# Kernel optimization log

Hardware: AMD Instinct MI355X
Metric: run time of the kernel (lower is better)

Reference implementation:

```python
import jax, jax.numpy as jnp
import numpy as np

B, T = 1024, 200
V = 100000   # item_size
H = 256      # hidden_size == embedding_size (GRU consumes embedding directly)
NUM_LAYERS = 2


def _gru_layer(x, w_ih, w_hh):
    """PyTorch GRU layer, bias=False. x: [B,T,in], w_ih: [3H,in], w_hh: [3H,H].
    Gate order in weights is (r, z, n)."""
    h0 = jnp.zeros((x.shape[0], w_hh.shape[1]), x.dtype)
    # Precompute all input projections in one big GEMM: [B,T,3H]
    x_proj = jnp.einsum('bti,gi->btg', x, w_ih)

    def step(h, xp):
        hp = h @ w_hh.T                      # [B,3H]
        xr, xz, xn = jnp.split(xp, 3, axis=-1)
        hr, hz, hn = jnp.split(hp, 3, axis=-1)
        r = jax.nn.sigmoid(xr + hr)
        z = jax.nn.sigmoid(xz + hz)
        n = jnp.tanh(xn + r * hn)
        h_new = (1.0 - z) * n + z * h
        return h_new, h_new

    _, ys = jax.lax.scan(step, h0, jnp.swapaxes(x_proj, 0, 1))  # [T,B,H]
    return jnp.swapaxes(ys, 0, 1)  # [B,T,H]


def setup_inputs() -> dict:
    key = jax.random.key(0)
    ks = jax.random.split(key, 8)
    input_ids = jax.random.randint(ks[0], (B, T), 0, V)
    s = 0.05
    emb = jax.random.normal(ks[1], (V, H), jnp.float32) * s
    emb = emb.at[0].set(0.0)  # padding_idx=0
    w_ih_l0 = jax.random.normal(ks[2], (3 * H, H), jnp.float32) * s
    w_hh_l0 = jax.random.normal(ks[3], (3 * H, H), jnp.float32) * s
    w_ih_l1 = jax.random.normal(ks[4], (3 * H, H), jnp.float32) * s
    w_hh_l1 = jax.random.normal(ks[5], (3 * H, H), jnp.float32) * s
    dense_w = jax.random.normal(ks[6], (H, H), jnp.float32) * s  # Linear(H, E=H)
    dense_b = jax.random.normal(ks[7], (H,), jnp.float32) * s
    return {"input_ids": input_ids, "emb": emb,
            "w_ih_l0": w_ih_l0, "w_hh_l0": w_hh_l0,
            "w_ih_l1": w_ih_l1, "w_hh_l1": w_hh_l1,
            "dense_w": dense_w, "dense_b": dense_b}


def reference(input_ids, emb, w_ih_l0, w_hh_l0, w_ih_l1, w_hh_l1, dense_w, dense_b):
    x = emb[input_ids]                 # [B,T,H] embedding lookup
    # emb_dropout is identity in eval mode
    x = _gru_layer(x, w_ih_l0, w_hh_l0)
    x = _gru_layer(x, w_ih_l1, w_hh_l1)
    return x @ dense_w.T + dense_b     # [B,T,H]
```

## Files before the change

### kernel.cpp

```cpp
#include <hip/hip_runtime.h>

#define T_LEN 200
#define HID   256
#define BATCH 1024
#define G3    768
#define ROWS  16
#define NTHREADS 512
#define WSZ   196608

typedef __bf16  bf16x8 __attribute__((ext_vector_type(8)));
typedef float   f32x4  __attribute__((ext_vector_type(4)));

__device__ __forceinline__ unsigned short f2bf(float f) {
  union { float f; unsigned int u; } c; c.f = f;
  unsigned int u = c.u;
  u += 0x7FFFu + ((u >> 16) & 1u);
  return (unsigned short)(u >> 16);
}
__device__ __forceinline__ float bf2f(unsigned int u16v) {
  union { unsigned int u; float f; } c; c.u = u16v << 16; return c.f;
}
__device__ __forceinline__ float sigm(float x) { return 1.0f / (1.0f + __expf(-x)); }
__device__ __forceinline__ float tanh_f(float x) { return 1.0f - 2.0f / (__expf(2.0f * x) + 1.0f); }

__global__ void convert_weights(const float* __restrict__ a,
                                const float* __restrict__ b,
                                const float* __restrict__ c,
                                const float* __restrict__ d,
                                const float* __restrict__ e,
                                unsigned short* __restrict__ out) {
  int i = blockIdx.x * blockDim.x + threadIdx.x;
  const int total = 4 * WSZ + HID * HID;
  if (i >= total) return;
  float v;
  if      (i < 1 * WSZ) v = a[i];
  else if (i < 2 * WSZ) v = b[i - 1 * WSZ];
  else if (i < 3 * WSZ) v = c[i - 2 * WSZ];
  else if (i < 4 * WSZ) v = d[i - 3 * WSZ];
  else                  v = e[i - 4 * WSZ];
  out[i] = f2bf(v);
}

__device__ __forceinline__ bf16x8 lds_frag(const unsigned short* buf, int row, int k, int lq) {
  int chunk = (k << 2) + lq;
  int idx = row * HID + ((chunk ^ (row & 7)) << 3);
  return *reinterpret_cast<const bf16x8*>(buf + idx);
}
__device__ __forceinline__ bf16x8 gw_frag(const unsigned short* __restrict__ W, int wrow, int kof) {
  return *reinterpret_cast<const bf16x8*>(W + (size_t)wrow * HID + kof);
}
__device__ __forceinline__ uint2 pack4(f32x4 v) {
  uint2 r;
  r.x = (unsigned int)f2bf(v[0]) | ((unsigned int)f2bf(v[1]) << 16);
  r.y = (unsigned int)f2bf(v[2]) | ((unsigned int)f2bf(v[3]) << 16);
  return r;
}

template<int GATHER>
__global__ __launch_bounds__(NTHREADS)
void xp_gemm(const int* __restrict__ ids, const float* __restrict__ emb,
             const unsigned short* __restrict__ hsrc,
             const unsigned short* __restrict__ W,
             unsigned short* __restrict__ xpT)
{
  __shared__ __align__(16) unsigned short As[128 * HID];
  const int tid = threadIdx.x;
  const int w = tid >> 6, lane = tid & 63, lr = lane & 15, lq = lane >> 4;
  const int bt = blockIdx.x & 63;
  const int tt = blockIdx.x >> 6;
  const int r0 = bt * 16, t0 = tt * 8;

  for (int idx = tid; idx < 128 * 32; idx += NTHREADS) {
    int row = idx >> 5, cc = idx & 31;
    int bloc = row & 15, tloc = row >> 4;
    int sidx = row * HID + ((cc ^ (row & 7)) << 3);
    if (GATHER) {
      int rid = ids[(r0 + bloc) * T_LEN + t0 + tloc];
      const f32x4* src = reinterpret_cast<const f32x4*>(emb + (size_t)rid * HID + cc * 8);
      f32x4 v0 = src[0], v1 = src[1];
      uint4 pk;
      pk.x = (unsigned int)f2bf(v0[0]) | ((unsigned int)f2bf(v0[1]) << 16);
      pk.y = (unsigned int)f2bf(v0[2]) | ((unsigned int)f2bf(v0[3]) << 16);
      pk.z = (unsigned int)f2bf(v1[0]) | ((unsigned int)f2bf(v1[1]) << 16);
      pk.w = (unsigned int)f2bf(v1[2]) | ((unsigned int)f2bf(v1[3]) << 16);
      *reinterpret_cast<uint4*>(&As[sidx]) = pk;
    } else {
      uint4 v = *reinterpret_cast<const uint4*>(hsrc + ((size_t)(r0 + bloc) * T_LEN + t0 + tloc) * HID + cc * 8);
      *reinterpret_cast<uint4*>(&As[sidx]) = v;
    }
  }
  __syncthreads();

  const int colbase = w * 96;
  #pragma unroll 1
  for (int mt = 0; mt < 8; ++mt) {
    bf16x8 a[8];
    #pragma unroll
    for (int k = 0; k < 8; ++k) a[k] = lds_frag(As, mt * 16 + lr, k, lq);
    const int t = t0 + mt;
    unsigned short* xprow = xpT + ((size_t)t * 64 + bt) * (G3 * 16);
    #pragma unroll
    for (int np = 0; np < 3; ++np) {
      const int c0 = colbase + np * 32;
      f32x4 acc0 = {0,0,0,0}, acc1 = {0,0,0,0};
      #pragma unroll
      for (int k = 0; k < 8; ++k) {
        const int kof = k * 32 + lq * 8;
        bf16x8 b0 = gw_frag(W, c0 + lr,      kof);
        bf16x8 b1 = gw_frag(W, c0 + 16 + lr, kof);
        acc0 = __builtin_amdgcn_mfma_f32_16x16x32_bf16(a[k], b0, acc0, 0, 0, 0);
        acc1 = __builtin_amdgcn_mfma_f32_16x16x32_bf16(a[k], b1, acc1, 0, 0, 0);
      }
      *reinterpret_cast<uint2*>(xprow + (c0 + lr)      * 16 + lq * 4) = pack4(acc0);
      *reinterpret_cast<uint2*>(xprow + (c0 + 16 + lr) * 16 + lq * 4) = pack4(acc1);
    }
  }
}

__global__ __launch_bounds__(NTHREADS, 2)
void gru_rec(const unsigned short* __restrict__ xpT,
             const unsigned short* __restrict__ Whh,
             unsigned short* __restrict__ hout)
{
  __shared__ __align__(16) unsigned short hb[2][ROWS * HID];
  const int tid = threadIdx.x;
  const int w = tid >> 6, lane = tid & 63, lr = lane & 15, lq = lane >> 4;
  const int bt = blockIdx.x;
  const int r0 = bt * ROWS;
  const int c0 = w * 32;

  bf16x8 wf[2][3][8];
  #pragma unroll
  for (int j = 0; j < 2; ++j)
    #pragma unroll
    for (int g = 0; g < 3; ++g)
      #pragma unroll
      for (int k = 0; k < 8; ++k)
        wf[j][g][k] = gw_frag(Whh, g * 256 + c0 + j * 16 + lr, k * 32 + lq * 8);

  for (int i = tid; i < ROWS * HID; i += NTHREADS) { hb[0][i] = 0; }

  f32x4 hreg[2] = {{0,0,0,0},{0,0,0,0}};

  const int bj0 = (c0 + lr) * 16 + lq * 4;
  const int bj1 = (c0 + 16 + lr) * 16 + lq * 4;

  const size_t slabstep = (size_t)64 * G3 * 16;
  const unsigned short* slab = xpT + (size_t)bt * (G3 * 16);

  __syncthreads();

  uint2 pz[2][3];
  #pragma unroll
  for (int g = 0; g < 3; ++g) {
    pz[0][g] = *reinterpret_cast<const uint2*>(slab + g * 4096 + bj0);
    pz[1][g] = *reinterpret_cast<const uint2*>(slab + g * 4096 + bj1);
  }

  int cur = 0;
  for (int t = 0; t < T_LEN; ++t) {
    f32x4 acc[2][3];
    uint2 xn0 = pz[0][2], xn1 = pz[1][2];
    #pragma unroll
    for (int j = 0; j < 2; ++j) {
      #pragma unroll
      for (int g = 0; g < 2; ++g) {
        uint2 p = pz[j][g];
        f32x4 v;
        v[0] = bf2f(p.x & 0xffffu); v[1] = bf2f(p.x >> 16);
        v[2] = bf2f(p.y & 0xffffu); v[3] = bf2f(p.y >> 16);
        acc[j][g] = v;
      }
      f32x4 z4 = {0,0,0,0};
      acc[j][2] = z4;
    }

    {
      const unsigned short* slab2 = (t + 1 < T_LEN) ? slab + slabstep : slab;
      #pragma unroll
      for (int g = 0; g < 3; ++g) {
        pz[0][g] = *reinterpret_cast<const uint2*>(slab2 + g * 4096 + bj0);
        pz[1][g] = *reinterpret_cast<const uint2*>(slab2 + g * 4096 + bj1);
      }
    }

    asm volatile("s_waitcnt lgkmcnt(0)\n\ts_barrier" ::: "memory");

    #pragma unroll
    for (int k = 0; k < 8; ++k) {
      bf16x8 a = lds_frag(hb[cur], lr, k, lq);
      #pragma unroll
      for (int j = 0; j < 2; ++j) {
        acc[j][0] = __builtin_amdgcn_mfma_f32_16x16x32_bf16(a, wf[j][0][k], acc[j][0], 0, 0, 0);
        acc[j][1] = __builtin_amdgcn_mfma_f32_16x16x32_bf16(a, wf[j][1][k], acc[j][1], 0, 0, 0);
        acc[j][2] = __builtin_amdgcn_mfma_f32_16x16x32_bf16(a, wf[j][2][k], acc[j][2], 0, 0, 0);
      }
    }

    #pragma unroll
    for (int j = 0; j < 2; ++j) {
      uint2 xn = j ? xn1 : xn0;
      float xnv[4];
      xnv[0] = bf2f(xn.x & 0xffffu); xnv[1] = bf2f(xn.x >> 16);
      xnv[2] = bf2f(xn.y & 0xffffu); xnv[3] = bf2f(xn.y >> 16);
      #pragma unroll
      for (int q = 0; q < 4; ++q) {
        float r = sigm(acc[j][0][q]);
        float z = sigm(acc[j][1][q]);
        float n = tanh_f(xnv[q] + r * acc[j][2][q]);
        float hnew = (1.0f - z) * n + z * hreg[j][q];
        hreg[j][q] = hnew;
        unsigned short hb16 = f2bf(hnew);
        int m = lq * 4 + q;
        int c = c0 + j * 16 + lr;
        hb[cur ^ 1][m * HID + (((c >> 3) ^ (m & 7)) << 3) + (c & 7)] = hb16;
        hout[((size_t)(r0 + m) * T_LEN + t) * HID + c] = hb16;
      }
    }
    slab += slabstep;
    cur ^= 1;
  }
}

__global__ __launch_bounds__(NTHREADS)
void dense_gemm(const unsigned short* __restrict__ hsrc,
                const unsigned short* __restrict__ Wd,
                const float* __restrict__ db,
                float* __restrict__ out)
{
  __shared__ __align__(16) unsigned short As[128 * HID];
  const int tid = threadIdx.x;
  const int w = tid >> 6, lane = tid & 63, lr = lane & 15, lq = lane >> 4;
  const int bt = blockIdx.x & 63;
  const int tt = blockIdx.x >> 6;
  const int r0 = bt * 16, t0 = tt * 8;

  for (int idx = tid; idx < 128 * 32; idx += NTHREADS) {
    int row = idx >> 5, cc = idx & 31;
    int bloc = row & 15, tloc = row >> 4;
    int sidx = row * HID + ((cc ^ (row & 7)) << 3);
    uint4 v = *reinterpret_cast<const uint4*>(hsrc + ((size_t)(r0 + bloc) * T_LEN + t0 + tloc) * HID + cc * 8);
    *reinterpret_cast<uint4*>(&As[sidx]) = v;
  }
  __syncthreads();

  const int c0 = w * 32;
  const float b0v = db[c0 + lr];
  const float b1v = db[c0 + 16 + lr];

  #pragma unroll 1
  for (int mt = 0; mt < 8; ++mt) {
    bf16x8 a[8];
    #pragma unroll
    for (int k = 0; k < 8; ++k) a[k] = lds_frag(As, mt * 16 + lr, k, lq);
    f32x4 acc0 = {0,0,0,0}, acc1 = {0,0,0,0};
    #pragma unroll
    for (int k = 0; k < 8; ++k) {
      const int kof = k * 32 + lq * 8;
      bf16x8 b0 = gw_frag(Wd, c0 + lr,      kof);
      bf16x8 b1 = gw_frag(Wd, c0 + 16 + lr, kof);
      acc0 = __builtin_amdgcn_mfma_f32_16x16x32_bf16(a[k], b0, acc0, 0, 0, 0);
      acc1 = __builtin_amdgcn_mfma_f32_16x16x32_bf16(a[k], b1, acc1, 0, 0, 0);
    }
    const int t = t0 + mt;
    #pragma unroll
    for (int q = 0; q < 4; ++q) {
      size_t base = ((size_t)(r0 + lq * 4 + q) * T_LEN + t) * HID;
      out[base + c0 + lr]      = acc0[q] + b0v;
      out[base + c0 + 16 + lr] = acc1[q] + b1v;
    }
  }
}

__device__ __forceinline__ void layer_step(
    const bf16x8* ax, const bf16x8* ah,
    const unsigned short* __restrict__ Wih,
    const unsigned short* __restrict__ Whh,
    float (&hreg)[2][4],
    unsigned short* __restrict__ outb,
    int c0base, int lr, int lq)
{
  #pragma unroll
  for (int j = 0; j < 2; ++j) {
    const int c0 = c0base + j * 16;
    f32x4 xr = {0,0,0,0}, xz = {0,0,0,0}, xn = {0,0,0,0};
    f32x4 hr = {0,0,0,0}, hz = {0,0,0,0}, hn = {0,0,0,0};
    #pragma unroll
    for (int k = 0; k < 8; ++k) {
      const int kof = k * 32 + lq * 8;
      bf16x8 b0 = gw_frag(Wih,       c0 + lr, kof);
      bf16x8 b1 = gw_frag(Wih, 256 + c0 + lr, kof);
      bf16x8 b2 = gw_frag(Wih, 512 + c0 + lr, kof);
      bf16x8 w0 = gw_frag(Whh,       c0 + lr, kof);
      bf16x8 w1 = gw_frag(Whh, 256 + c0 + lr, kof);
      bf16x8 w2 = gw_frag(Whh, 512 + c0 + lr, kof);
      xr = __builtin_amdgcn_mfma_f32_16x16x32_bf16(ax[k], b0, xr, 0, 0, 0);
      xz = __builtin_amdgcn_mfma_f32_16x16x32_bf16(ax[k], b1, xz, 0, 0, 0);
      xn = __builtin_amdgcn_mfma_f32_16x16x32_bf16(ax[k], b2, xn, 0, 0, 0);
      hr = __builtin_amdgcn_mfma_f32_16x16x32_bf16(ah[k], w0, hr, 0, 0, 0);
      hz = __builtin_amdgcn_mfma_f32_16x16x32_bf16(ah[k], w1, hz, 0, 0, 0);
      hn = __builtin_amdgcn_mfma_f32_16x16x32_bf16(ah[k], w2, hn, 0, 0, 0);
    }
    #pragma unroll
    for (int q = 0; q < 4; ++q) {
      float r = sigm(xr[q] + hr[q]);
      float z = sigm(xz[q] + hz[q]);
      float n = tanh_f(xn[q] + r * hn[q]);
      float h = (1.0f - z) * n + z * hreg[j][q];
      hreg[j][q] = h;
      int m = lq * 4 + q;
      int c = c0 + lr;
      int idx = m * HID + (((c >> 3) ^ (m & 7)) << 3) + (c & 7);
      outb[idx] = f2bf(h);
    }
  }
}

__global__ __launch_bounds__(NTHREADS)
void gru_fused(const int* __restrict__ ids,
               const float* __restrict__ emb,
               const unsigned short* __restrict__ wbf,
               const float* __restrict__ dense_b,
               float* __restrict__ out)
{
  __shared__ __align__(16) unsigned short x_bf[ROWS * HID];
  __shared__ __align__(16) unsigned short h0b[2][ROWS * HID];
  __shared__ __align__(16) unsigned short h1b[2][ROWS * HID];

  const int tid  = threadIdx.x;
  const int w    = tid >> 6;
  const int lane = tid & 63;
  const int lr   = lane & 15;
  const int lq   = lane >> 4;
  const int r0   = blockIdx.x * ROWS;
  const int c0base = w * 32;

  const unsigned short* Wih0 = wbf;
  const unsigned short* Whh0 = wbf + 1 * WSZ;
  const unsigned short* Wih1 = wbf + 2 * WSZ;
  const unsigned short* Whh1 = wbf + 3 * WSZ;
  const unsigned short* Wd   = wbf + 4 * WSZ;

  for (int i = tid; i < ROWS * HID; i += NTHREADS) {
    h0b[0][i] = 0; h0b[1][i] = 0; h1b[0][i] = 0; h1b[1][i] = 0;
  }
  float hreg0[2][4] = {}; float hreg1[2][4] = {};
  const float bias0 = dense_b[c0base + lr];
  const float bias1 = dense_b[c0base + 16 + lr];

  const int grow   = tid >> 5;
  const int gchunk = tid & 31;
  const int gswz   = grow * HID + ((gchunk ^ (grow & 7)) << 3);
  const int gid_base = (r0 + grow) * T_LEN;

  __syncthreads();

  int cur = 0;
  for (int t = 0; t < T_LEN; ++t) {
    {
      int rid = ids[gid_base + t];
      const f32x4* src = reinterpret_cast<const f32x4*>(emb + (size_t)rid * HID + gchunk * 8);
      f32x4 v0 = src[0];
      f32x4 v1 = src[1];
      uint4 pk;
      pk.x = (unsigned int)f2bf(v0[0]) | ((unsigned int)f2bf(v0[1]) << 16);
      pk.y = (unsigned int)f2bf(v0[2]) | ((unsigned int)f2bf(v0[3]) << 16);
      pk.z = (unsigned int)f2bf(v1[0]) | ((unsigned int)f2bf(v1[1]) << 16);
      pk.w = (unsigned int)f2bf(v1[2]) | ((unsigned int)f2bf(v1[3]) << 16);
      *reinterpret_cast<uint4*>(&x_bf[gswz]) = pk;
    }
    __syncthreads();

    bf16x8 ax[8], ah[8];
    #pragma unroll
    for (int k = 0; k < 8; ++k) {
      ax[k] = lds_frag(x_bf,     lr, k, lq);
      ah[k] = lds_frag(h0b[cur], lr, k, lq);
    }
    layer_step(ax, ah, Wih0, Whh0, hreg0, h0b[cur ^ 1], c0base, lr, lq);
    __syncthreads();

    #pragma unroll
    for (int k = 0; k < 8; ++k) {
      ax[k] = lds_frag(h0b[cur ^ 1], lr, k, lq);
      ah[k] = lds_frag(h1b[cur],     lr, k, lq);
    }
    layer_step(ax, ah, Wih1, Whh1, hreg1, h1b[cur ^ 1], c0base, lr, lq);
    __syncthreads();

    #pragma unroll
    for (int k = 0; k < 8; ++k) ax[k] = lds_frag(h1b[cur ^ 1], lr, k, lq);
    #pragma unroll
    for (int j = 0; j < 2; ++j) {
      const int c0 = c0base + j * 16;
      f32x4 acc = {0,0,0,0};
      #pragma unroll
      for (int k = 0; k < 8; ++k) {
        bf16x8 bw = gw_frag(Wd, c0 + lr, k * 32 + lq * 8);
        acc = __builtin_amdgcn_mfma_f32_16x16x32_bf16(ax[k], bw, acc, 0, 0, 0);
      }
      const float bias = j ? bias1 : bias0;
      size_t base = ((size_t)(r0 + lq * 4) * T_LEN + t) * HID + c0 + lr;
      #pragma unroll
      for (int q = 0; q < 4; ++q) {
        out[base + (size_t)q * T_LEN * HID] = acc[q] + bias;
      }
    }
    cur ^= 1;
  }
}

extern "C" void kernel_launch(void* const* d_in, const int* in_sizes, int n_in,
                              void* d_out, int out_size, void* d_ws, size_t ws_size,
                              hipStream_t stream) {
  const int*   ids  = (const int*)d_in[0];
  const float* emb  = (const float*)d_in[1];
  const float* wih0 = (const float*)d_in[2];
  const float* whh0 = (const float*)d_in[3];
  const float* wih1 = (const float*)d_in[4];
  const float* whh1 = (const float*)d_in[5];
  const float* dw   = (const float*)d_in[6];
  const float* db   = (const float*)d_in[7];

  unsigned short* wbf = (unsigned short*)d_ws;

  const int total = 4 * WSZ + HID * HID;
  convert_weights<<<(total + 255) / 256, 256, 0, stream>>>(wih0, whh0, wih1, whh1, dw, wbf);

  const size_t XP_OFF = 2u * 1024u * 1024u;
  const size_t XP_BYTES = (size_t)T_LEN * G3 * BATCH * 2;
  const size_t H_OFF  = XP_OFF + XP_BYTES;
  const size_t H_BYTES = (size_t)BATCH * T_LEN * HID * 2;
  const size_t NEED = H_OFF + H_BYTES;

  if (ws_size >= NEED) {
    unsigned short* xpT  = (unsigned short*)((char*)d_ws + XP_OFF);
    unsigned short* hbuf = (unsigned short*)((char*)d_ws + H_OFF);
    const unsigned short* Wih0 = wbf;
    const unsigned short* Whh0 = wbf + 1 * WSZ;
    const unsigned short* Wih1 = wbf + 2 * WSZ;
    const unsigned short* Whh1 = wbf + 3 * WSZ;
    const unsigned short* Wd   = wbf + 4 * WSZ;

    xp_gemm<1><<<1600, NTHREADS, 0, stream>>>(ids, emb, nullptr, Wih0, xpT);
    gru_rec<<<64, NTHREADS, 0, stream>>>(xpT, Whh0, hbuf);
    xp_gemm<0><<<1600, NTHREADS, 0, stream>>>(nullptr, nullptr, hbuf, Wih1, xpT);
    gru_rec<<<64, NTHREADS, 0, stream>>>(xpT, Whh1, hbuf);
    dense_gemm<<<1600, NTHREADS, 0, stream>>>(hbuf, Wd, db, (float*)d_out);
  } else {
    gru_fused<<<64, NTHREADS, 0, stream>>>(ids, emb, wbf, db, (float*)d_out);
  }
}
```

Before: 2.432 ms.

## Split GRU recurrence across 16 waves with one 16-column tile each

The recurrent kernel now runs 1024 threads (16 waves) per block instead of 512, and each wave owns a single 16-column slice of the hidden state rather than two. This halves the per-wave MFMA chain and gate math on the serial per-timestep critical path, and halves the per-wave register footprint for the resident W_hh fragments. An empty asm pins those fragments in VGPRs. In exchange, the per-step barrier has to synchronize twice as many waves. The launch-bounds occupancy hint is also raised.

```diff
diff --git a/kernel.cpp b/kernel.cpp
--- a/kernel.cpp
+++ b/kernel.cpp
@@ -6,6 +6,7 @@
 #define G3    768
 #define ROWS  16
 #define NTHREADS 512
+#define RECTHREADS 1024
 #define WSZ   196608
 
 typedef __bf16  bf16x8 __attribute__((ext_vector_type(8)));
@@ -49,6 +50,10 @@
 __device__ __forceinline__ bf16x8 gw_frag(const unsigned short* __restrict__ W, int wrow, int kof) {
   return *reinterpret_cast<const bf16x8*>(W + (size_t)wrow * HID + kof);
 }
+__device__ __forceinline__ uint4 gw_fragu(const unsigned short* __restrict__ W, int wrow, int kof) {
+  return *reinterpret_cast<const uint4*>(W + (size_t)wrow * HID + kof);
+}
+__device__ __forceinline__ bf16x8 as_bf(uint4 u) { return __builtin_bit_cast(bf16x8, u); }
 __device__ __forceinline__ uint2 pack4(f32x4 v) {
   uint2 r;
   r.x = (unsigned int)f2bf(v[0]) | ((unsigned int)f2bf(v[1]) << 16);
@@ -117,7 +122,7 @@
   }
 }
 
-__global__ __launch_bounds__(NTHREADS, 2)
+__global__ __launch_bounds__(RECTHREADS, 4)
 void gru_rec(const unsigned short* __restrict__ xpT,
              const unsigned short* __restrict__ Whh,
              unsigned short* __restrict__ hout)
@@ -127,61 +132,57 @@
   const int w = tid >> 6, lane = tid & 63, lr = lane & 15, lq = lane >> 4;
   const int bt = blockIdx.x;
   const int r0 = bt * ROWS;
-  const int c0 = w * 32;
-
-  bf16x8 wf[2][3][8];
+  const int c0 = w * 16;
+
+  uint4 wf[3][8];
   #pragma unroll
-  for (int j = 0; j < 2; ++j)
-    #pragma unroll
-    for (int g = 0; g < 3; ++g)
-      #pragma unroll
-      for (int k = 0; k < 8; ++k)
-        wf[j][g][k] = gw_frag(Whh, g * 256 + c0 + j * 16 + lr, k * 32 + lq * 8);
-
-  for (int i = tid; i < ROWS * HID; i += NTHREADS) { hb[0][i] = 0; }
-
-  f32x4 hreg[2] = {{0,0,0,0},{0,0,0,0}};
-
-  const int bj0 = (c0 + lr) * 16 + lq * 4;
-  const int bj1 = (c0 + 16 + lr) * 16 + lq * 4;
+  for (int g = 0; g < 3; ++g)
+    #pragma unroll
+    for (int k = 0; k < 8; ++k)
+      wf[g][k] = gw_fragu(Whh, g * 256 + c0 + lr, k * 32 + lq * 8);
+  #pragma unroll
+  for (int g = 0; g < 3; ++g)
+    #pragma unroll
+    for (int k = 0; k < 8; ++k)
+      asm volatile("" : "+v"(wf[g][k].x), "+v"(wf[g][k].y),
+                        "+v"(wf[g][k].z), "+v"(wf[g][k].w));
+
+  for (int i = tid; i < ROWS * HID; i += RECTHREADS) { hb[0][i] = 0; }
+
+  f32x4 hreg = {0, 0, 0, 0};
+
+  const int bj = (c0 + lr) * 16 + lq * 4;
 
   const size_t slabstep = (size_t)64 * G3 * 16;
   const unsigned short* slab = xpT + (size_t)bt * (G3 * 16);
 
   __syncthreads();
 
-  uint2 pz[2][3];
+  uint2 pz[3];
   #pragma unroll
-  for (int g = 0; g < 3; ++g) {
-    pz[0][g] = *reinterpret_cast<const uint2*>(slab + g * 4096 + bj0);
-    pz[1][g] = *reinterpret_cast<const uint2*>(slab + g * 4096 + bj1);
-  }
+  for (int g = 0; g < 3; ++g)
+    pz[g] = *reinterpret_cast<const uint2*>(slab + g * 4096 + bj);
 
   int cur = 0;
+  #pragma unroll 1
   for (int t = 0; t < T_LEN; ++t) {
-    f32x4 acc[2][3];
-    uint2 xn0 = pz[0][2], xn1 = pz[1][2];
-    #pragma unroll
-    for (int j = 0; j < 2; ++j) {
-      #pragma unroll
-      for (int g = 0; g < 2; ++g) {
-        uint2 p = pz[j][g];
-        f32x4 v;
-        v[0] = bf2f(p.x & 0xffffu); v[1] = bf2f(p.x >> 16);
-        v[2] = bf2f(p.y & 0xffffu); v[3] = bf2f(p.y >> 16);
-        acc[j][g] = v;
-      }
-      f32x4 z4 = {0,0,0,0};
-      acc[j][2] = z4;
-    }
+    f32x4 acc[3];
+    uint2 xn = pz[2];
+    #pragma unroll
+    for (int g = 0; g < 2; ++g) {
+      uint2 p = pz[g];
+      f32x4 v;
+      v[0] = bf2f(p.x & 0xffffu); v[1] = bf2f(p.x >> 16);
+      v[2] = bf2f(p.y & 0xffffu); v[3] = bf2f(p.y >> 16);
+      acc[g] = v;
+    }
+    { f32x4 z4 = {0,0,0,0}; acc[2] = z4; }
 
     {
       const unsigned short* slab2 = (t + 1 < T_LEN) ? slab + slabstep : slab;
       #pragma unroll
-      for (int g = 0; g < 3; ++g) {
-        pz[0][g] = *reinterpret_cast<const uint2*>(slab2 + g * 4096 + bj0);
-        pz[1][g] = *reinterpret_cast<const uint2*>(slab2 + g * 4096 + bj1);
-      }
+      for (int g = 0; g < 3; ++g)
+        pz[g] = *reinterpret_cast<const uint2*>(slab2 + g * 4096 + bj);
     }
 
     asm volatile("s_waitcnt lgkmcnt(0)\n\ts_barrier" ::: "memory");
@@ -189,30 +190,25 @@
     #pragma unroll
     for (int k = 0; k < 8; ++k) {
       bf16x8 a = lds_frag(hb[cur], lr, k, lq);
-      #pragma unroll
-      for (int j = 0; j < 2; ++j) {
-        acc[j][0] = __builtin_amdgcn_mfma_f32_16x16x32_bf16(a, wf[j][0][k], acc[j][0], 0, 0, 0);
-        acc[j][1] = __builtin_amdgcn_mfma_f32_16x16x32_bf16(a, wf[j][1][k], acc[j][1], 0, 0, 0);
-        acc[j][2] = __builtin_amdgcn_mfma_f32_16x16x32_bf16(a, wf[j][2][k], acc[j][2], 0, 0, 0);
-      }
-    }
-
-    #pragma unroll
-    for (int j = 0; j < 2; ++j) {
-      uint2 xn = j ? xn1 : xn0;
+      acc[0] = __builtin_amdgcn_mfma_f32_16x16x32_bf16(a, as_bf(wf[0][k]), acc[0], 0, 0, 0);
+      acc[1] = __builtin_amdgcn_mfma_f32_16x16x32_bf16(a, as_bf(wf[1][k]), acc[1], 0, 0, 0);
+      acc[2] = __builtin_amdgcn_mfma_f32_16x16x32_bf16(a, as_bf(wf[2][k]), acc[2], 0, 0, 0);
+    }
+
+    {
       float xnv[4];
       xnv[0] = bf2f(xn.x & 0xffffu); xnv[1] = bf2f(xn.x >> 16);
       xnv[2] = bf2f(xn.y & 0xffffu); xnv[3] = bf2f(xn.y >> 16);
+      const int c = c0 + lr;
       #pragma unroll
       for (int q = 0; q < 4; ++q) {
-        float r = sigm(acc[j][0][q]);
-        float z = sigm(acc[j][1][q]);
-        float n = tanh_f(xnv[q] + r * acc[j][2][q]);
-        float hnew = (1.0f - z) * n + z * hreg[j][q];
-        hreg[j][q] = hnew;
+        float r = sigm(acc[0][q]);
+        float z = sigm(acc[1][q]);
+        float n = tanh_f(xnv[q] + r * acc[2][q]);
+        float hnew = (1.0f - z) * n + z * hreg[q];
+        hreg[q] = hnew;
         unsigned short hb16 = f2bf(hnew);
         int m = lq * 4 + q;
-        int c = c0 + j * 16 + lr;
         hb[cur ^ 1][m * HID + (((c >> 3) ^ (m & 7)) << 3) + (c & 7)] = hb16;
         hout[((size_t)(r0 + m) * T_LEN + t) * HID + c] = hb16;
       }
@@ -443,9 +439,9 @@
     const unsigned short* Wd   = wbf + 4 * WSZ;
 
     xp_gemm<1><<<1600, NTHREADS, 0, stream>>>(ids, emb, nullptr, Wih0, xpT);
-    gru_rec<<<64, NTHREADS, 0, stream>>>(xpT, Whh0, hbuf);
+    gru_rec<<<64, RECTHREADS, 0, stream>>>(xpT, Whh0, hbuf);
     xp_gemm<0><<<1600, NTHREADS, 0, stream>>>(nullptr, nullptr, hbuf, Wih1, xpT);
-    gru_rec<<<64, NTHREADS, 0, stream>>>(xpT, Whh1, hbuf);
+    gru_rec<<<64, RECTHREADS, 0, stream>>>(xpT, Whh1, hbuf);
     dense_gemm<<<1600, NTHREADS, 0, stream>>>(hbuf, Wd, db, (float*)d_out);
   } else {
     gru_fused<<<64, NTHREADS, 0, stream>>>(ids, emb, wbf, db, (float*)d_out);
```

Result: slower. 2.510 ms (+3.2%).

## Fuse GRU stages into persistent megakernel with flag-based producer/consumer pipelining

Applied to the files above, without the earlier changes.

Replaces five separate launches (input-projection GEMM, layer-0 recurrence, layer-1 projection, layer-1 recurrence, dense GEMM) with one persistent kernel of 256 blocks. The blocks are split into four roles that hand off 8-timestep granules through global flags and cache-coherent stores and loads. This lets the layer-0 and layer-1 recurrences and the surrounding GEMMs run concurrently instead of back to back. The hidden-state buffer is re-laid out per timestep slab to match the swizzled LDS layout. The design depends on all 256 blocks being co-resident, otherwise it deadlocks, and coherent loads and stores add latency to each step. The output update is also rewritten as a single fmaf.

```diff
diff --git a/kernel.cpp b/kernel.cpp
--- a/kernel.cpp
+++ b/kernel.cpp
@@ -7,6 +7,7 @@
 #define ROWS  16
 #define NTHREADS 512
 #define WSZ   196608
+#define NGRAN 25
 
 typedef __bf16  bf16x8 __attribute__((ext_vector_type(8)));
 typedef float   f32x4  __attribute__((ext_vector_type(4)));
@@ -56,25 +57,78 @@
   return r;
 }
 
-template<int GATHER>
-__global__ __launch_bounds__(NTHREADS)
-void xp_gemm(const int* __restrict__ ids, const float* __restrict__ emb,
-             const unsigned short* __restrict__ hsrc,
-             const unsigned short* __restrict__ W,
-             unsigned short* __restrict__ xpT)
-{
-  __shared__ __align__(16) unsigned short As[128 * HID];
-  const int tid = threadIdx.x;
+__device__ __forceinline__ uint2 ld_u2_sys(const unsigned short* p) {
+  unsigned long long v = __hip_atomic_load(
+      reinterpret_cast<const unsigned long long*>(p),
+      __ATOMIC_RELAXED, __HIP_MEMORY_SCOPE_SYSTEM);
+  uint2 r; r.x = (unsigned int)v; r.y = (unsigned int)(v >> 32);
+  return r;
+}
+__device__ __forceinline__ void st_u2_coh(unsigned short* p, uint2 v) {
+  asm volatile("global_store_dwordx2 %0, %1, off sc0 sc1" :: "v"(p), "v"(v) : "memory");
+}
+__device__ __forceinline__ void st_sh_coh(unsigned short* p, unsigned int v) {
+  asm volatile("global_store_short %0, %1, off sc0 sc1" :: "v"(p), "v"(v) : "memory");
+}
+
+__device__ __forceinline__ void flag_wait(int* f, int tid) {
+  if (tid == 0) {
+    while (!__hip_atomic_load(f, __ATOMIC_ACQUIRE, __HIP_MEMORY_SCOPE_AGENT))
+      __builtin_amdgcn_s_sleep(2);
+  }
+  __syncthreads();
+}
+__device__ __forceinline__ void flag_set(int* f, int tid) {
+  asm volatile("s_waitcnt vmcnt(0)" ::: "memory");
+  __syncthreads();
+  if (tid == 0) __hip_atomic_store(f, 1, __ATOMIC_RELEASE, __HIP_MEMORY_SCOPE_AGENT);
+}
+
+__device__ __forceinline__ void xp_mfma_store(
+    const unsigned short* As, const unsigned short* __restrict__ W,
+    unsigned short* __restrict__ xpT, int bt, int t0, int w, int lr, int lq)
+{
+  const int colbase = w * 96;
+  #pragma unroll 1
+  for (int mt = 0; mt < 8; ++mt) {
+    bf16x8 a[8];
+    #pragma unroll
+    for (int k = 0; k < 8; ++k) a[k] = lds_frag(As, mt * 16 + lr, k, lq);
+    unsigned short* xprow = xpT + ((size_t)(t0 + mt) * 64 + bt) * (G3 * 16);
+    #pragma unroll
+    for (int np = 0; np < 3; ++np) {
+      const int c0 = colbase + np * 32;
+      f32x4 acc0 = {0,0,0,0}, acc1 = {0,0,0,0};
+      #pragma unroll
+      for (int k = 0; k < 8; ++k) {
+        const int kof = k * 32 + lq * 8;
+        bf16x8 b0 = gw_frag(W, c0 + lr,      kof);
+        bf16x8 b1 = gw_frag(W, c0 + 16 + lr, kof);
+        acc0 = __builtin_amdgcn_mfma_f32_16x16x32_bf16(a[k], b0, acc0, 0, 0, 0);
+        acc1 = __builtin_amdgcn_mfma_f32_16x16x32_bf16(a[k], b1, acc1, 0, 0, 0);
+      }
+      st_u2_coh(xprow + (c0 + lr)      * 16 + lq * 4, pack4(acc0));
+      st_u2_coh(xprow + (c0 + 16 + lr) * 16 + lq * 4, pack4(acc1));
+    }
+  }
+}
+
+__device__ __forceinline__ void role_b(
+    const int* __restrict__ ids, const float* __restrict__ emb,
+    const unsigned short* __restrict__ Wih0, const unsigned short* __restrict__ Wih1,
+    unsigned short* __restrict__ xpT, const unsigned short* __restrict__ hbuf,
+    int* flagZ, int* flagA, int* flagB,
+    unsigned short* As, int bt, int tid)
+{
   const int w = tid >> 6, lane = tid & 63, lr = lane & 15, lq = lane >> 4;
-  const int bt = blockIdx.x & 63;
-  const int tt = blockIdx.x >> 6;
-  const int r0 = bt * 16, t0 = tt * 8;
-
-  for (int idx = tid; idx < 128 * 32; idx += NTHREADS) {
-    int row = idx >> 5, cc = idx & 31;
-    int bloc = row & 15, tloc = row >> 4;
-    int sidx = row * HID + ((cc ^ (row & 7)) << 3);
-    if (GATHER) {
+  const int r0 = bt * 16;
+
+  for (int gt = 0; gt < NGRAN; ++gt) {
+    const int t0 = gt * 8;
+    for (int idx = tid; idx < 128 * 32; idx += NTHREADS) {
+      int row = idx >> 5, cc = idx & 31;
+      int bloc = row & 15, tloc = row >> 4;
+      int sidx = row * HID + ((cc ^ (row & 7)) << 3);
       int rid = ids[(r0 + bloc) * T_LEN + t0 + tloc];
       const f32x4* src = reinterpret_cast<const f32x4*>(emb + (size_t)rid * HID + cc * 8);
       f32x4 v0 = src[0], v1 = src[1];
@@ -84,50 +138,41 @@
       pk.z = (unsigned int)f2bf(v1[0]) | ((unsigned int)f2bf(v1[1]) << 16);
       pk.w = (unsigned int)f2bf(v1[2]) | ((unsigned int)f2bf(v1[3]) << 16);
       *reinterpret_cast<uint4*>(&As[sidx]) = pk;
-    } else {
-      uint4 v = *reinterpret_cast<const uint4*>(hsrc + ((size_t)(r0 + bloc) * T_LEN + t0 + tloc) * HID + cc * 8);
+    }
+    __syncthreads();
+    xp_mfma_store(As, Wih0, xpT, bt, t0, w, lr, lq);
+    flag_set(flagZ + gt, tid);
+  }
+
+  for (int gt = 0; gt < NGRAN; ++gt) {
+    flag_wait(flagA + gt, tid);
+    for (int idx = tid; idx < 128 * 32; idx += NTHREADS) {
+      int row = idx >> 5, cc = idx & 31;
+      int bloc = row & 15, tloc = row >> 4;
+      int sidx = row * HID + ((cc ^ (row & 7)) << 3);
+      const unsigned short* hs = hbuf + ((size_t)(gt * 8 + tloc) * 64 + bt) * (ROWS * HID)
+                                      + bloc * HID + ((cc ^ (bloc & 7)) << 3);
+      uint2 v0 = ld_u2_sys(hs);
+      uint2 v1 = ld_u2_sys(hs + 4);
+      uint4 v; v.x = v0.x; v.y = v0.y; v.z = v1.x; v.w = v1.y;
       *reinterpret_cast<uint4*>(&As[sidx]) = v;
     }
-  }
-  __syncthreads();
-
-  const int colbase = w * 96;
-  #pragma unroll 1
-  for (int mt = 0; mt < 8; ++mt) {
-    bf16x8 a[8];
-    #pragma unroll
-    for (int k = 0; k < 8; ++k) a[k] = lds_frag(As, mt * 16 + lr, k, lq);
-    const int t = t0 + mt;
-    unsigned short* xprow = xpT + ((size_t)t * 64 + bt) * (G3 * 16);
-    #pragma unroll
-    for (int np = 0; np < 3; ++np) {
-      const int c0 = colbase + np * 32;
-      f32x4 acc0 = {0,0,0,0}, acc1 = {0,0,0,0};
-      #pragma unroll
-      for (int k = 0; k < 8; ++k) {
-        const int kof = k * 32 + lq * 8;
-        bf16x8 b0 = gw_frag(W, c0 + lr,      kof);
-        bf16x8 b1 = gw_frag(W, c0 + 16 + lr, kof);
-        acc0 = __builtin_amdgcn_mfma_f32_16x16x32_bf16(a[k], b0, acc0, 0, 0, 0);
-        acc1 = __builtin_amdgcn_mfma_f32_16x16x32_bf16(a[k], b1, acc1, 0, 0, 0);
-      }
-      *reinterpret_cast<uint2*>(xprow + (c0 + lr)      * 16 + lq * 4) = pack4(acc0);
-      *reinterpret_cast<uint2*>(xprow + (c0 + 16 + lr) * 16 + lq * 4) = pack4(acc1);
-    }
-  }
-}
-
-__global__ __launch_bounds__(NTHREADS, 2)
-void gru_rec(const unsigned short* __restrict__ xpT,
-             const unsigned short* __restrict__ Whh,
-             unsigned short* __restrict__ hout)
-{
-  __shared__ __align__(16) unsigned short hb[2][ROWS * HID];
-  const int tid = threadIdx.x;
+    __syncthreads();
+    xp_mfma_store(As, Wih1, xpT, bt, gt * 8, w, lr, lq);
+    flag_set(flagB + gt, tid);
+  }
+}
+
+__device__ __forceinline__ void role_rec(
+    const unsigned short* __restrict__ xpT,
+    const unsigned short* __restrict__ Whh,
+    unsigned short* __restrict__ hbuf,
+    int* inflag, int* outflag,
+    unsigned short* smem, int bt, int tid)
+{
   const int w = tid >> 6, lane = tid & 63, lr = lane & 15, lq = lane >> 4;
-  const int bt = blockIdx.x;
-  const int r0 = bt * ROWS;
   const int c0 = w * 32;
+  unsigned short* hb = smem;
 
   bf16x8 wf[2][3][8];
   #pragma unroll
@@ -138,137 +183,176 @@
       for (int k = 0; k < 8; ++k)
         wf[j][g][k] = gw_frag(Whh, g * 256 + c0 + j * 16 + lr, k * 32 + lq * 8);
 
-  for (int i = tid; i < ROWS * HID; i += NTHREADS) { hb[0][i] = 0; }
-
+  for (int i = tid; i < 2 * ROWS * HID; i += NTHREADS) hb[i] = 0;
   f32x4 hreg[2] = {{0,0,0,0},{0,0,0,0}};
-
   const int bj0 = (c0 + lr) * 16 + lq * 4;
-  const int bj1 = (c0 + 16 + lr) * 16 + lq * 4;
-
   const size_t slabstep = (size_t)64 * G3 * 16;
-  const unsigned short* slab = xpT + (size_t)bt * (G3 * 16);
-
   __syncthreads();
 
+  int cur = 0;
   uint2 pz[2][3];
-  #pragma unroll
-  for (int g = 0; g < 3; ++g) {
-    pz[0][g] = *reinterpret_cast<const uint2*>(slab + g * 4096 + bj0);
-    pz[1][g] = *reinterpret_cast<const uint2*>(slab + g * 4096 + bj1);
-  }
-
-  int cur = 0;
-  for (int t = 0; t < T_LEN; ++t) {
-    f32x4 acc[2][3];
-    uint2 xn0 = pz[0][2], xn1 = pz[1][2];
-    #pragma unroll
-    for (int j = 0; j < 2; ++j) {
-      #pragma unroll
-      for (int g = 0; g < 2; ++g) {
-        uint2 p = pz[j][g];
-        f32x4 v;
-        v[0] = bf2f(p.x & 0xffffu); v[1] = bf2f(p.x >> 16);
-        v[2] = bf2f(p.y & 0xffffu); v[3] = bf2f(p.y >> 16);
-        acc[j][g] = v;
-      }
-      f32x4 z4 = {0,0,0,0};
-      acc[j][2] = z4;
-    }
-
-    {
-      const unsigned short* slab2 = (t + 1 < T_LEN) ? slab + slabstep : slab;
-      #pragma unroll
-      for (int g = 0; g < 3; ++g) {
-        pz[0][g] = *reinterpret_cast<const uint2*>(slab2 + g * 4096 + bj0);
-        pz[1][g] = *reinterpret_cast<const uint2*>(slab2 + g * 4096 + bj1);
-      }
-    }
-
-    asm volatile("s_waitcnt lgkmcnt(0)\n\ts_barrier" ::: "memory");
-
-    #pragma unroll
-    for (int k = 0; k < 8; ++k) {
-      bf16x8 a = lds_frag(hb[cur], lr, k, lq);
+  #pragma unroll 1
+  for (int gt = 0; gt < NGRAN; ++gt) {
+    flag_wait(inflag + gt, tid);
+    const unsigned short* slab = xpT + ((size_t)(gt * 8) * 64 + bt) * (G3 * 16);
+    #pragma unroll
+    for (int g = 0; g < 3; ++g) {
+      pz[0][g] = ld_u2_sys(slab + g * 4096 + bj0);
+      pz[1][g] = ld_u2_sys(slab + g * 4096 + bj0 + 256);
+    }
+    #pragma unroll 1
+    for (int s = 0; s < 8; ++s) {
+      const int t = gt * 8 + s;
+
+      f32x4 acc[2][3];
+      uint2 xn0 = pz[0][2], xn1 = pz[1][2];
       #pragma unroll
       for (int j = 0; j < 2; ++j) {
-        acc[j][0] = __builtin_amdgcn_mfma_f32_16x16x32_bf16(a, wf[j][0][k], acc[j][0], 0, 0, 0);
-        acc[j][1] = __builtin_amdgcn_mfma_f32_16x16x32_bf16(a, wf[j][1][k], acc[j][1], 0, 0, 0);
-        acc[j][2] = __builtin_amdgcn_mfma_f32_16x16x32_bf16(a, wf[j][2][k], acc[j][2], 0, 0, 0);
-      }
-    }
-
-    #pragma unroll
-    for (int j = 0; j < 2; ++j) {
-      uint2 xn = j ? xn1 : xn0;
-      float xnv[4];
-      xnv[0] = bf2f(xn.x & 0xffffu); xnv[1] = bf2f(xn.x >> 16);
-      xnv[2] = bf2f(xn.y & 0xffffu); xnv[3] = bf2f(xn.y >> 16);
-      #pragma unroll
-      for (int q = 0; q < 4; ++q) {
-        float r = sigm(acc[j][0][q]);
-        float z = sigm(acc[j][1][q]);
-        float n = tanh_f(xnv[q] + r * acc[j][2][q]);
-        float hnew = (1.0f - z) * n + z * hreg[j][q];
-        hreg[j][q] = hnew;
-        unsigned short hb16 = f2bf(hnew);
-        int m = lq * 4 + q;
-        int c = c0 + j * 16 + lr;
-        hb[cur ^ 1][m * HID + (((c >> 3) ^ (m & 7)) << 3) + (c & 7)] = hb16;
-        hout[((size_t)(r0 + m) * T_LEN + t) * HID + c] = hb16;
-      }
-    }
-    slab += slabstep;
-    cur ^= 1;
-  }
-}
-
-__global__ __launch_bounds__(NTHREADS)
-void dense_gemm(const unsigned short* __restrict__ hsrc,
-                const unsigned short* __restrict__ Wd,
-                const float* __restrict__ db,
-                float* __restrict__ out)
-{
-  __shared__ __align__(16) unsigned short As[128 * HID];
-  const int tid = threadIdx.x;
+        #pragma unroll
+        for (int g = 0; g < 2; ++g) {
+          uint2 p = pz[j][g];
+          f32x4 v;
+          v[0] = bf2f(p.x & 0xffffu); v[1] = bf2f(p.x >> 16);
+          v[2] = bf2f(p.y & 0xffffu); v[3] = bf2f(p.y >> 16);
+          acc[j][g] = v;
+        }
+        f32x4 z4 = {0,0,0,0};
+        acc[j][2] = z4;
+      }
+      if (s < 7) {
+        const unsigned short* slab2 = slab + slabstep;
+        #pragma unroll
+        for (int g = 0; g < 3; ++g) {
+          pz[0][g] = ld_u2_sys(slab2 + g * 4096 + bj0);
+          pz[1][g] = ld_u2_sys(slab2 + g * 4096 + bj0 + 256);
+        }
+      }
+      asm volatile("s_waitcnt lgkmcnt(0)\ns_barrier" ::: "memory");
+
+      const unsigned short* hbc = hb + cur * (ROWS * HID);
+      #pragma unroll
+      for (int k = 0; k < 8; ++k) {
+        bf16x8 a = lds_frag(hbc, lr, k, lq);
+        #pragma unroll
+        for (int j = 0; j < 2; ++j) {
+          acc[j][0] = __builtin_amdgcn_mfma_f32_16x16x32_bf16(a, wf[j][0][k], acc[j][0], 0, 0, 0);
+          acc[j][1] = __builtin_amdgcn_mfma_f32_16x16x32_bf16(a, wf[j][1][k], acc[j][1], 0, 0, 0);
+          acc[j][2] = __builtin_amdgcn_mfma_f32_16x16x32_bf16(a, wf[j][2][k], acc[j][2], 0, 0, 0);
+        }
+      }
+
+      unsigned short* hbn = hb + (cur ^ 1) * (ROWS * HID);
+      unsigned short* hslab = hbuf + ((size_t)t * 64 + bt) * (ROWS * HID);
+      #pragma unroll
+      for (int j = 0; j < 2; ++j) {
+        uint2 xn = j ? xn1 : xn0;
+        float xnv[4];
+        xnv[0] = bf2f(xn.x & 0xffffu); xnv[1] = bf2f(xn.x >> 16);
+        xnv[2] = bf2f(xn.y & 0xffffu); xnv[3] = bf2f(xn.y >> 16);
+        #pragma unroll
+        for (int q = 0; q < 4; ++q) {
+          float r = sigm(acc[j][0][q]);
+          float z = sigm(acc[j][1][q]);
+          float n = tanh_f(xnv[q] + r * acc[j][2][q]);
+          float hnew = fmaf(z, hreg[j][q] - n, n);
+          hreg[j][q] = hnew;
+          unsigned short h16 = f2bf(hnew);
+          int m = lq * 4 + q;
+          int c = c0 + j * 16 + lr;
+          int off = m * HID + (((c >> 3) ^ (m & 7)) << 3) + (c & 7);
+          hbn[off] = h16;
+          st_sh_coh(hslab + off, (unsigned int)h16);
+        }
+      }
+      slab += slabstep;
+      cur ^= 1;
+    }
+    flag_set(outflag + gt, tid);
+  }
+}
+
+__device__ __forceinline__ void role_d(
+    const unsigned short* __restrict__ hbuf,
+    const unsigned short* __restrict__ Wd, const float* __restrict__ db,
+    float* __restrict__ out, int* flagC,
+    unsigned short* As, int bt, int tid)
+{
   const int w = tid >> 6, lane = tid & 63, lr = lane & 15, lq = lane >> 4;
-  const int bt = blockIdx.x & 63;
-  const int tt = blockIdx.x >> 6;
-  const int r0 = bt * 16, t0 = tt * 8;
-
-  for (int idx = tid; idx < 128 * 32; idx += NTHREADS) {
-    int row = idx >> 5, cc = idx & 31;
-    int bloc = row & 15, tloc = row >> 4;
-    int sidx = row * HID + ((cc ^ (row & 7)) << 3);
-    uint4 v = *reinterpret_cast<const uint4*>(hsrc + ((size_t)(r0 + bloc) * T_LEN + t0 + tloc) * HID + cc * 8);
-    *reinterpret_cast<uint4*>(&As[sidx]) = v;
-  }
-  __syncthreads();
-
+  const int r0 = bt * 16;
   const int c0 = w * 32;
   const float b0v = db[c0 + lr];
   const float b1v = db[c0 + 16 + lr];
 
-  #pragma unroll 1
-  for (int mt = 0; mt < 8; ++mt) {
-    bf16x8 a[8];
-    #pragma unroll
-    for (int k = 0; k < 8; ++k) a[k] = lds_frag(As, mt * 16 + lr, k, lq);
-    f32x4 acc0 = {0,0,0,0}, acc1 = {0,0,0,0};
-    #pragma unroll
-    for (int k = 0; k < 8; ++k) {
-      const int kof = k * 32 + lq * 8;
-      bf16x8 b0 = gw_frag(Wd, c0 + lr,      kof);
-      bf16x8 b1 = gw_frag(Wd, c0 + 16 + lr, kof);
-      acc0 = __builtin_amdgcn_mfma_f32_16x16x32_bf16(a[k], b0, acc0, 0, 0, 0);
-      acc1 = __builtin_amdgcn_mfma_f32_16x16x32_bf16(a[k], b1, acc1, 0, 0, 0);
-    }
-    const int t = t0 + mt;
-    #pragma unroll
-    for (int q = 0; q < 4; ++q) {
-      size_t base = ((size_t)(r0 + lq * 4 + q) * T_LEN + t) * HID;
-      out[base + c0 + lr]      = acc0[q] + b0v;
-      out[base + c0 + 16 + lr] = acc1[q] + b1v;
-    }
+  for (int gt = 0; gt < NGRAN; ++gt) {
+    flag_wait(flagC + gt, tid);
+    for (int idx = tid; idx < 128 * 32; idx += NTHREADS) {
+      int row = idx >> 5, cc = idx & 31;
+      int bloc = row & 15, tloc = row >> 4;
+      int sidx = row * HID + ((cc ^ (row & 7)) << 3);
+      const unsigned short* hs = hbuf + ((size_t)(gt * 8 + tloc) * 64 + bt) * (ROWS * HID)
+                                      + bloc * HID + ((cc ^ (bloc & 7)) << 3);
+      uint2 v0 = ld_u2_sys(hs);
+      uint2 v1 = ld_u2_sys(hs + 4);
+      uint4 v; v.x = v0.x; v.y = v0.y; v.z = v1.x; v.w = v1.y;
+      *reinterpret_cast<uint4*>(&As[sidx]) = v;
+    }
+    __syncthreads();
+    #pragma unroll 1
+    for (int mt = 0; mt < 8; ++mt) {
+      bf16x8 a[8];
+      #pragma unroll
+      for (int k = 0; k < 8; ++k) a[k] = lds_frag(As, mt * 16 + lr, k, lq);
+      f32x4 acc0 = {0,0,0,0}, acc1 = {0,0,0,0};
+      #pragma unroll
+      for (int k = 0; k < 8; ++k) {
+        const int kof = k * 32 + lq * 8;
+        bf16x8 b0 = gw_frag(Wd, c0 + lr,      kof);
+        bf16x8 b1 = gw_frag(Wd, c0 + 16 + lr, kof);
+        acc0 = __builtin_amdgcn_mfma_f32_16x16x32_bf16(a[k], b0, acc0, 0, 0, 0);
+        acc1 = __builtin_amdgcn_mfma_f32_16x16x32_bf16(a[k], b1, acc1, 0, 0, 0);
+      }
+      const int t = gt * 8 + mt;
+      #pragma unroll
+      for (int q = 0; q < 4; ++q) {
+        size_t base = ((size_t)(r0 + lq * 4 + q) * T_LEN + t) * HID;
+        out[base + c0 + lr]      = acc0[q] + b0v;
+        out[base + c0 + 16 + lr] = acc1[q] + b1v;
+      }
+    }
+    __syncthreads();
+  }
+}
+
+__global__ __launch_bounds__(NTHREADS)
+void mega(const int* __restrict__ ids, const float* __restrict__ emb,
+          const unsigned short* __restrict__ wbf, const float* __restrict__ db,
+          unsigned short* __restrict__ xpT, unsigned short* __restrict__ hbuf,
+          int* __restrict__ flags, float* __restrict__ out)
+{
+  __shared__ __align__(16) unsigned short smem[128 * HID];
+  const int role = blockIdx.x >> 6;
+  const int bt   = blockIdx.x & 63;
+  const int tid  = threadIdx.x;
+
+  const unsigned short* Wih0 = wbf;
+  const unsigned short* Whh0 = wbf + 1 * WSZ;
+  const unsigned short* Wih1 = wbf + 2 * WSZ;
+  const unsigned short* Whh1 = wbf + 3 * WSZ;
+  const unsigned short* Wd   = wbf + 4 * WSZ;
+
+  int* flagZ = flags + (0 * 64 + bt) * NGRAN;
+  int* flagA = flags + (1 * 64 + bt) * NGRAN;
+  int* flagB = flags + (2 * 64 + bt) * NGRAN;
+  int* flagC = flags + (3 * 64 + bt) * NGRAN;
+
+  if (role == 0) {
+    role_b(ids, emb, Wih0, Wih1, xpT, hbuf, flagZ, flagA, flagB, smem, bt, tid);
+  } else if (role == 1) {
+    role_rec(xpT, Whh0, hbuf, flagZ, flagA, smem, bt, tid);
+  } else if (role == 2) {
+    role_rec(xpT, Whh1, hbuf, flagB, flagC, smem, bt, tid);
+  } else {
+    role_d(hbuf, Wd, db, out, flagC, smem, bt, tid);
   }
 }
 
@@ -306,7 +390,7 @@
       float r = sigm(xr[q] + hr[q]);
       float z = sigm(xz[q] + hz[q]);
       float n = tanh_f(xn[q] + r * hn[q]);
-      float h = (1.0f - z) * n + z * hreg[j][q];
+      float h = fmaf(z, hreg[j][q] - n, n);
       hreg[j][q] = h;
       int m = lq * 4 + q;
       int c = c0 + lr;
@@ -427,26 +511,20 @@
   const int total = 4 * WSZ + HID * HID;
   convert_weights<<<(total + 255) / 256, 256, 0, stream>>>(wih0, whh0, wih1, whh1, dw, wbf);
 
-  const size_t XP_OFF = 2u * 1024u * 1024u;
+  const size_t FLAGS_OFF  = 1835008;
+  const size_t FLAG_BYTES = 4 * 64 * NGRAN * sizeof(int);
+  const size_t XP_OFF   = 2u * 1024u * 1024u;
   const size_t XP_BYTES = (size_t)T_LEN * G3 * BATCH * 2;
-  const size_t H_OFF  = XP_OFF + XP_BYTES;
-  const size_t H_BYTES = (size_t)BATCH * T_LEN * HID * 2;
-  const size_t NEED = H_OFF + H_BYTES;
+  const size_t H_OFF    = XP_OFF + XP_BYTES;
+  const size_t H_BYTES  = (size_t)BATCH * T_LEN * HID * 2;
+  const size_t NEED     = H_OFF + H_BYTES;
 
   if (ws_size >= NEED) {
     unsigned short* xpT  = (unsigned short*)((char*)d_ws + XP_OFF);
     unsigned short* hbuf = (unsigned short*)((char*)d_ws + H_OFF);
-    const unsigned short* Wih0 = wbf;
-    const unsigned short* Whh0 = wbf + 1 * WSZ;
-    const unsigned short* Wih1 = wbf + 2 * WSZ;
-    const unsigned short* Whh1 = wbf + 3 * WSZ;
-    const unsigned short* Wd   = wbf + 4 * WSZ;
-
-    xp_gemm<1><<<1600, NTHREADS, 0, stream>>>(ids, emb, nullptr, Wih0, xpT);
-    gru_rec<<<64, NTHREADS, 0, stream>>>(xpT, Whh0, hbuf);
-    xp_gemm<0><<<1600, NTHREADS, 0, stream>>>(nullptr, nullptr, hbuf, Wih1, xpT);
-    gru_rec<<<64, NTHREADS, 0, stream>>>(xpT, Whh1, hbuf);
-    dense_gemm<<<1600, NTHREADS, 0, stream>>>(hbuf, Wd, db, (float*)d_out);
+    int* flags = (int*)((char*)d_ws + FLAGS_OFF);
+    hipMemsetAsync(flags, 0, FLAG_BYTES, stream);
+    mega<<<256, NTHREADS, 0, stream>>>(ids, emb, wbf, db, xpT, hbuf, flags, (float*)d_out);
   } else {
     gru_fused<<<64, NTHREADS, 0, stream>>>(ids, emb, wbf, db, (float*)d_out);
   }
```

New measurement: 9.062 ms. 3.73x slower.
